# Kernel optimization log

Measured on AMD Instinct MI355X. Metric: run time of the kernel, lower is better.

The kernel has to match this reference:

```python
import jax, jax.numpy as jnp
import numpy as np

# MLA dims (DeepSeek-V3-lite style)
B, S, DIM = 1, 2048, 2048
H, NOPE, ROPE, VD, LORA = 16, 128, 64, 128, 512
QK_HEAD = NOPE + ROPE  # 192
SCALE = QK_HEAD ** -0.5
EPS = 1e-6


def _rmsnorm(x, w):
    return x * jax.lax.rsqrt(jnp.mean(x * x, axis=-1, keepdims=True) + EPS) * w


def _apply_rope(x, cos, sin):
    # x: [b, s, h, d] with interleaved (real, imag) pairs; cos/sin: [s, d//2]
    x0, x1 = x[..., 0::2], x[..., 1::2]
    c = cos[None, :, None, :]
    s = sin[None, :, None, :]
    y0 = x0 * c - x1 * s
    y1 = x0 * s + x1 * c
    return jnp.stack([y0, y1], axis=-1).reshape(x.shape)


def setup_inputs() -> dict:
    key = jax.random.key(0)
    ks = jax.random.split(key, 6)
    x = jax.random.normal(ks[0], (B, S, DIM), jnp.float32) * 0.02
    wq = jax.random.normal(ks[1], (H * QK_HEAD, DIM), jnp.float32) * 0.02
    wkv_a = jax.random.normal(ks[2], (LORA + ROPE, DIM), jnp.float32) * 0.02
    kv_norm_w = jnp.ones((LORA,), jnp.float32)
    wkv_b = jax.random.normal(ks[3], (H * (NOPE + VD), LORA), jnp.float32) * 0.02
    wo = jax.random.normal(ks[4], (DIM, H * VD), jnp.float32) * 0.02
    # rotary freqs_cis (cos/sin) for qk_rope_head_dim
    inv_freq = 1.0 / (10000.0 ** (np.arange(0, ROPE, 2, dtype=np.float32) / ROPE))
    t = np.arange(S, dtype=np.float32)
    ang = np.outer(t, inv_freq)  # [S, ROPE//2]
    cos = jnp.asarray(np.cos(ang), jnp.float32)
    sin = jnp.asarray(np.sin(ang), jnp.float32)
    return {"x": x, "cos": cos, "sin": sin, "wq": wq, "wkv_a": wkv_a,
            "kv_norm_w": kv_norm_w, "wkv_b": wkv_b, "wo": wo}


def reference(x, cos, sin, wq, wkv_a, kv_norm_w, wkv_b, wo):
    b, s, _ = x.shape
    # queries
    q = (x @ wq.T).reshape(b, s, H, QK_HEAD)
    q_nope, q_pe = q[..., :NOPE], q[..., NOPE:]
    q_pe = _apply_rope(q_pe, cos, sin)  # [b,s,h,rope]
    # latent kv
    kv = x @ wkv_a.T  # [b,s,lora+rope]
    kv_c, k_pe = kv[..., :LORA], kv[..., LORA:]
    k_pe = _apply_rope(k_pe[:, :, None, :], cos, sin)[:, :, 0, :]  # [b,s,rope]
    kv_c = _rmsnorm(kv_c, kv_norm_w)  # latent kv cache [b,s,lora]
    # absorbed weights: wkv_b viewed as [h, nope+vd, lora]
    wkv_b_r = wkv_b.reshape(H, NOPE + VD, LORA)
    w_uk = wkv_b_r[:, :NOPE]   # [h, nope, lora]
    w_uv = wkv_b_r[:, NOPE:]   # [h, vd, lora]
    # absorb: project q_nope into latent space
    q_c = jnp.einsum('bshd,hdc->bshc', q_nope, w_uk)  # [b,s,h,lora]
    scores = (jnp.einsum('bshc,btc->bsht', q_c, kv_c)
              + jnp.einsum('bshr,btr->bsht', q_pe, k_pe)) * SCALE
    # causal mask over [s, t]
    mask = jnp.where(jnp.arange(s)[:, None] >= jnp.arange(s)[None, :], 0.0, -1e30)
    scores = scores + mask[None, :, None, :].astype(scores.dtype)
    attn = jax.nn.softmax(scores, axis=-1)
    o = jnp.einsum('bsht,btc->bshc', attn, kv_c)       # [b,s,h,lora]
    o = jnp.einsum('bshc,hdc->bshd', o, w_uv)           # [b,s,h,vd]
    out = o.reshape(b, s, H * VD) @ wo.T                # [b,s,dim]
    return out
```

## Files before the change

### kernel.cpp

```cpp
#include <hip/hip_runtime.h>
#include <hip/hip_bf16.h>
#include <math.h>

#define S_LEN 2048
#define DIM   2048
#define H_N   16
#define NOPE  128
#define ROPE  64
#define VD    128
#define LORA  512
#define D_QK  576
#define SCALE_F 0.07216878364870323f
#define EPS_F 1e-6f
#define KVF 640
#define KVS 1280

typedef short short8 __attribute__((ext_vector_type(8)));
typedef short short4v __attribute__((ext_vector_type(4)));
typedef float floatx4 __attribute__((ext_vector_type(4)));

static __device__ inline unsigned short f2bf_bits(float f) {
  union { __hip_bfloat16 h; unsigned short u; } cv;
  cv.h = __float2bfloat16(f);
  return cv.u;
}

static __device__ inline float bf2f(unsigned short b) {
  union { unsigned u; float f; } cv;
  cv.u = (unsigned)b << 16;
  return cv.f;
}

static __device__ inline void gload_lds16(const short* gptr, short* lds_base_uniform) {
  __builtin_amdgcn_global_load_lds(
      (const __attribute__((address_space(1))) void*)gptr,
      (__attribute__((address_space(3))) void*)lds_base_uniform, 16, 0, 0);
}

__global__ __launch_bounds__(256) void cast_f32_bf16(
    const float* __restrict__ src, short* __restrict__ dst, int n8) {
  int i = blockIdx.x * 256 + threadIdx.x;
  if (i < n8) {
    float4 a = ((const float4*)src)[2 * i];
    float4 b = ((const float4*)src)[2 * i + 1];
    uint4 o;
    o.x = (unsigned)f2bf_bits(a.x) | ((unsigned)f2bf_bits(a.y) << 16);
    o.y = (unsigned)f2bf_bits(a.z) | ((unsigned)f2bf_bits(a.w) << 16);
    o.z = (unsigned)f2bf_bits(b.x) | ((unsigned)f2bf_bits(b.y) << 16);
    o.w = (unsigned)f2bf_bits(b.z) | ((unsigned)f2bf_bits(b.w) << 16);
    ((uint4*)dst)[i] = o;
  }
}

__global__ __launch_bounds__(256) void zero_short8(short* __restrict__ dst, int n8) {
  int i = blockIdx.x * 256 + threadIdx.x;
  if (i < n8) ((uint4*)dst)[i] = (uint4){0u, 0u, 0u, 0u};
}

__global__ __launch_bounds__(256) void transpose_wuk(
    const float* __restrict__ wkvb, short* __restrict__ wukT) {
  __shared__ float tile[32][33];
  const int h = blockIdx.z, c0 = blockIdx.y * 32, d0 = blockIdx.x * 32;
  const int t = threadIdx.x;
  const int r = t >> 3, c4 = (t & 7) * 4;
  float4 v = *(const float4*)(wkvb + ((long)h * 256 + d0 + r) * 512 + c0 + c4);
  tile[r][c4 + 0] = v.x; tile[r][c4 + 1] = v.y;
  tile[r][c4 + 2] = v.z; tile[r][c4 + 3] = v.w;
  __syncthreads();
  uint2 o;
  o.x = (unsigned)f2bf_bits(tile[c4 + 0][r]) | ((unsigned)f2bf_bits(tile[c4 + 1][r]) << 16);
  o.y = (unsigned)f2bf_bits(tile[c4 + 2][r]) | ((unsigned)f2bf_bits(tile[c4 + 3][r]) << 16);
  *(uint2*)(wukT + ((long)h * 512 + c0 + r) * 128 + d0 + c4) = o;
}

__global__ __launch_bounds__(256) void gemm_bf16_nt(
    const short* __restrict__ A, const short* __restrict__ B, void* __restrict__ Cv,
    int K, int lda, int ldb, int ldc, long aB, long bB, long cB, int bf16out) {
  A += (long)blockIdx.z * aB;
  B += (long)blockIdx.z * bB;
  const int m0 = blockIdx.y * 128, n0 = blockIdx.x * 128;
  __shared__ short As[2][128 * 32];
  __shared__ short Bs[2][128 * 32];
  const int tid = threadIdx.x, w = tid >> 6, lane = tid & 63;
  const int ln = lane & 15, g = lane >> 4;
  const int mw = (w & 1) * 64, nw = (w >> 1) * 64;
  floatx4 acc[4][4];
#pragma unroll
  for (int i = 0; i < 4; ++i)
#pragma unroll
    for (int j = 0; j < 4; ++j) acc[i][j] = (floatx4){0.f, 0.f, 0.f, 0.f};

#define GEMM_STAGE(k0_, b_)                                                    \
  {                                                                            \
    _Pragma("unroll")                                                          \
    for (int i = 0; i < 2; ++i) {                                              \
      const int bc = (i * 4 + w) * 64;                                         \
      const int c = bc + lane;                                                 \
      const int row = c >> 2, quar = c & 3;                                    \
      gload_lds16(A + (long)(m0 + row) * lda + (k0_) + quar * 8, As[b_] + bc * 8); \
      gload_lds16(B + (long)(n0 + row) * ldb + (k0_) + quar * 8, Bs[b_] + bc * 8); \
    }                                                                          \
  }

  GEMM_STAGE(0, 0);
  __syncthreads();
  const int nk = K >> 5;
  for (int kt = 0; kt < nk; ++kt) {
    const int cb = kt & 1;
    if (kt + 1 < nk) GEMM_STAGE((kt + 1) << 5, cb ^ 1);
    short8 af[4], bf_[4];
#pragma unroll
    for (int mi = 0; mi < 4; ++mi)
      af[mi] = *(const short8*)(As[cb] + (mw + mi * 16 + ln) * 32 + g * 8);
#pragma unroll
    for (int ni = 0; ni < 4; ++ni)
      bf_[ni] = *(const short8*)(Bs[cb] + (nw + ni * 16 + ln) * 32 + g * 8);
#pragma unroll
    for (int mi = 0; mi < 4; ++mi)
#pragma unroll
      for (int ni = 0; ni < 4; ++ni)
        acc[mi][ni] = __builtin_amdgcn_mfma_f32_16x16x32_bf16(af[mi], bf_[ni], acc[mi][ni], 0, 0, 0);
    __syncthreads();
  }
#undef GEMM_STAGE
  if (bf16out) {
    short* Cs = (short*)Cv + (long)blockIdx.z * cB;
#pragma unroll
    for (int mi = 0; mi < 4; ++mi)
#pragma unroll
      for (int ni = 0; ni < 4; ++ni)
#pragma unroll
        for (int r = 0; r < 4; ++r)
          Cs[(long)(m0 + mw + mi * 16 + g * 4 + r) * ldc + n0 + nw + ni * 16 + ln] =
              (short)f2bf_bits(acc[mi][ni][r]);
  } else {
    float* C = (float*)Cv + (long)blockIdx.z * cB;
#pragma unroll
    for (int mi = 0; mi < 4; ++mi)
#pragma unroll
      for (int ni = 0; ni < 4; ++ni)
#pragma unroll
        for (int r = 0; r < 4; ++r)
          C[(long)(m0 + mw + mi * 16 + g * 4 + r) * ldc + n0 + nw + ni * 16 + ln] = acc[mi][ni][r];
  }
}

__global__ __launch_bounds__(64) void prep_kernel(
    float* kv, const short* __restrict__ qbufb, short* __restrict__ qhatb,
    const float* __restrict__ cosp, const float* __restrict__ sinp,
    const float* __restrict__ normw) {
  const int s = blockIdx.x;
  const int l = threadIdx.x;
  float* row = kv + (long)s * KVF;
  short* krow = (short*)kv + (long)s * KVS;

  float4 v0 = *(const float4*)(row + l * 8);
  float4 v1 = *(const float4*)(row + l * 8 + 4);
  float rx0 = 0.f, rx1 = 0.f, rc = 0.f, rs = 0.f;
  if (l < 32) {
    rc = cosp[s * 32 + l];
    rs = sinp[s * 32 + l];
    rx0 = row[512 + 2 * l];
    rx1 = row[512 + 2 * l + 1];
  }
  float4 w0 = *(const float4*)(normw + l * 8);
  float4 w1 = *(const float4*)(normw + l * 8 + 4);

  float ss = v0.x * v0.x + v0.y * v0.y + v0.z * v0.z + v0.w * v0.w +
             v1.x * v1.x + v1.y * v1.y + v1.z * v1.z + v1.w * v1.w;
#pragma unroll
  for (int off = 32; off; off >>= 1) ss += __shfl_xor(ss, off, 64);
  const float scale = rsqrtf(ss * (1.0f / (float)LORA) + EPS_F);
  v0.x *= scale * w0.x; v0.y *= scale * w0.y; v0.z *= scale * w0.z; v0.w *= scale * w0.w;
  v1.x *= scale * w1.x; v1.y *= scale * w1.y; v1.z *= scale * w1.z; v1.w *= scale * w1.w;

  uint4 pk;
  pk.x = (unsigned)f2bf_bits(v0.x) | ((unsigned)f2bf_bits(v0.y) << 16);
  pk.y = (unsigned)f2bf_bits(v0.z) | ((unsigned)f2bf_bits(v0.w) << 16);
  pk.z = (unsigned)f2bf_bits(v1.x) | ((unsigned)f2bf_bits(v1.y) << 16);
  pk.w = (unsigned)f2bf_bits(v1.z) | ((unsigned)f2bf_bits(v1.w) << 16);
  *(uint4*)(krow + l * 8) = pk;

  if (l < 32) {
    const float y0 = rx0 * rc - rx1 * rs;
    const float y1 = rx0 * rs + rx1 * rc;
    unsigned pr = (unsigned)f2bf_bits(y0) | ((unsigned)f2bf_bits(y1) << 16);
    *(unsigned*)(krow + 512 + 2 * l) = pr;
  }

#pragma unroll
  for (int it = 0; it < 8; ++it) {
    const int p = it * 64 + l;
    const int h = p >> 5;
    const int i = p & 31;
    const float c = cosp[s * 32 + i];
    const float sn = sinp[s * 32 + i];
    const short* qp = qbufb + (long)s * 3072 + h * 192 + NOPE;
    const unsigned uq = *(const unsigned*)(qp + 2 * i);
    const float x0 = bf2f((unsigned short)uq);
    const float x1 = bf2f((unsigned short)(uq >> 16));
    const float y0 = x0 * c - x1 * sn;
    const float y1 = x0 * sn + x1 * c;
    short* dst = qhatb + ((long)h * S_LEN + s) * D_QK + 512;
    *(unsigned*)(dst + 2 * i) = (unsigned)f2bf_bits(y0) | ((unsigned)f2bf_bits(y1) << 16);
  }
}

__global__ __launch_bounds__(256) void transpose_v(
    const short* __restrict__ kbf, short* __restrict__ kvt) {
  __shared__ short tile[32][36];
  const int d0 = blockIdx.x * 32;
  const int s0 = blockIdx.y * 32;
  const int t = threadIdx.x;
  const int r = t >> 3;
  const int c4 = (t & 7) * 4;
  uint2 v = *(const uint2*)(kbf + (long)(s0 + r) * KVS + d0 + c4);
  *(uint2*)(&tile[r][c4]) = v;
  __syncthreads();
  uint2 o;
  o.x = (unsigned)(unsigned short)tile[c4 + 0][r] | ((unsigned)(unsigned short)tile[c4 + 1][r] << 16);
  o.y = (unsigned)(unsigned short)tile[c4 + 2][r] | ((unsigned)(unsigned short)tile[c4 + 3][r] << 16);
  *(uint2*)(kvt + (long)(d0 + r) * S_LEN + s0 + c4) = o;
}

__global__ __launch_bounds__(256) void build_ktt(
    const short* __restrict__ kbf, short* __restrict__ ktt) {
  const int kt = blockIdx.x;
  for (int idx = threadIdx.x; idx < 18 * 64; idx += 256) {
    const int c = idx >> 6, l = idx & 63;
    const int ln = l & 15, g = l >> 4;
    uint4 v = *(const uint4*)(kbf + (long)(kt * 16 + ln) * KVS + c * 32 + g * 8);
    *(uint4*)(ktt + ((long)(kt * 18 + c) * 64 + l) * 8) = v;
  }
}

__global__ __launch_bounds__(256) void build_vtt(
    const short* __restrict__ kvt, short* __restrict__ vtt) {
  const int kt = blockIdx.x;
  for (int idx = threadIdx.x; idx < 32 * 64; idx += 256) {
    const int nt = idx >> 6, l = idx & 63;
    const int ln = l & 15, g = l >> 4;
    uint4 v = *(const uint4*)(kvt + (long)(nt * 16 + ln) * S_LEN + kt * 32 + g * 8);
    *(uint4*)(vtt + ((long)(kt * 32 + nt) * 64 + l) * 8) = v;
  }
}

__global__ __launch_bounds__(256, 2) void flash_reg(
    const short* __restrict__ qhat,
    const short* __restrict__ ktt,
    const short* __restrict__ vtt,
    short* __restrict__ obuf) {
  const int bid = blockIdx.x;
  const int hp = bid & 7;
  const int v = bid >> 3;
  const int vi = v & 31, vj = v >> 5;
  const int qw = (vj == 0) ? 127 - vi : (vj == 1) ? 64 + vi : (vj == 2) ? 63 - vi : vi;
  const int q0 = qw * 16;
  const int tid = threadIdx.x;
  const int w = tid >> 6;
  const int lane = tid & 63;
  const int ln = lane & 15, g = lane >> 4;
  const int hh = w & 1;
  const int h = hp * 2 + hh;
  const int dh = w >> 1;
  const int vbase = dh * 256;
  const int qlim = q0 + ln;

  __shared__ short Kt[2][36 * 64 * 8];
  __shared__ __align__(16) short Pl[2][2][16][40];
  __shared__ float Ls[4][16];

  short8 qfr[18];
  {
    const short* qrow = qhat + ((long)h * S_LEN + q0 + ln) * D_QK;
#pragma unroll
    for (int c = 0; c < 18; ++c)
      qfr[c] = *(const short8*)(qrow + c * 32 + g * 8);
  }

  floatx4 oacc[16];
#pragma unroll
  for (int nt = 0; nt < 16; ++nt) oacc[nt] = (floatx4){0.f, 0.f, 0.f, 0.f};
  float lsum = 0.f;

  const int npairs = (qw + 2) >> 1;

#define FL_STAGE(pair_, b_)                                                    \
  {                                                                            \
    const short* ksrc_ = ktt + (long)(pair_) * (36 * 512);                     \
    _Pragma("unroll")                                                          \
    for (int i = 0; i < 9; ++i) {                                              \
      const int grp = i * 4 + w;                                               \
      gload_lds16(ksrc_ + (long)(grp * 64 + lane) * 8, Kt[b_] + grp * 512);    \
    }                                                                          \
  }

#define FL_PV(pp_, par_)                                                       \
  {                                                                            \
    const short8 pb8 = *(const short8*)(&Pl[par_][hh][ln][g * 8]);             \
    const short* vp = vtt + (((long)(pp_) * 32 + dh * 16) * 64 + lane) * 8;    \
    _Pragma("unroll")                                                          \
    for (int half = 0; half < 2; ++half) {                                     \
      short8 va[8];                                                            \
      _Pragma("unroll")                                                        \
      for (int j = 0; j < 8; ++j)                                              \
        va[j] = *(const short8*)(vp + (half * 8 + j) * 512);                   \
      __builtin_amdgcn_s_setprio(1);                                           \
      _Pragma("unroll")                                                        \
      for (int j = 0; j < 8; ++j)                                              \
        oacc[half * 8 + j] = __builtin_amdgcn_mfma_f32_16x16x32_bf16(          \
            va[j], pb8, oacc[half * 8 + j], 0, 0, 0);                          \
      __builtin_amdgcn_s_setprio(0);                                           \
    }                                                                          \
  }

  FL_STAGE(0, 0);
  __syncthreads();

  for (int p = 0; p < npairs; ++p) {
    const int cb = p & 1;
    if (p + 1 < npairs) FL_STAGE(p + 1, cb ^ 1);
    const int t0 = p * 32;
    const short* kb = Kt[cb] + dh * (18 * 512);
    floatx4 s0 = (floatx4){0.f, 0.f, 0.f, 0.f};
    floatx4 s1 = (floatx4){0.f, 0.f, 0.f, 0.f};
    __builtin_amdgcn_s_setprio(1);
#pragma unroll
    for (int c = 0; c < 18; c += 2) {
      short8 k0 = *(const short8*)(kb + (c * 64 + lane) * 8);
      short8 k1 = *(const short8*)(kb + ((c + 1) * 64 + lane) * 8);
      s0 = __builtin_amdgcn_mfma_f32_16x16x32_bf16(k0, qfr[c], s0, 0, 0, 0);
      s1 = __builtin_amdgcn_mfma_f32_16x16x32_bf16(k1, qfr[c + 1], s1, 0, 0, 0);
    }
    __builtin_amdgcn_s_setprio(0);
    short4v p4;
    float psum = 0.f;
#pragma unroll
    for (int r = 0; r < 4; ++r) {
      const int ki = t0 + dh * 16 + g * 4 + r;
      float sc = fminf(fmaxf((s0[r] + s1[r]) * SCALE_F, -30.f), 30.f);
      float pv_ = (ki <= qlim) ? __expf(sc) : 0.f;
      psum += pv_;
      p4[r] = (short)f2bf_bits(pv_);
    }
    lsum += psum;
    union { short4v s; unsigned long long u; } upk;
    upk.s = p4;
    *(unsigned long long*)(&Pl[cb][hh][ln][dh * 16 + g * 4]) = upk.u;
    if (p > 0) FL_PV(p - 1, cb ^ 1);
    __syncthreads();
  }
  FL_PV(npairs - 1, (npairs - 1) & 1);
#undef FL_PV
#undef FL_STAGE

  lsum += __shfl_xor(lsum, 16, 64);
  lsum += __shfl_xor(lsum, 32, 64);
  if (g == 0) Ls[w][ln] = lsum;
  __syncthreads();
  lsum += Ls[w ^ 2][ln];
  const float inv = 1.0f / fmaxf(lsum, 1e-30f);

  short* orow = obuf + ((long)h * S_LEN + q0 + ln) * 512 + vbase + g * 4;
#pragma unroll
  for (int nt = 0; nt < 16; ++nt) {
    unsigned lo = (unsigned)f2bf_bits(oacc[nt][0] * inv) | ((unsigned)f2bf_bits(oacc[nt][1] * inv) << 16);
    unsigned hi = (unsigned)f2bf_bits(oacc[nt][2] * inv) | ((unsigned)f2bf_bits(oacc[nt][3] * inv) << 16);
    unsigned long long st = (unsigned long long)lo | ((unsigned long long)hi << 32);
    *(unsigned long long*)(orow + nt * 16) = st;
  }
}

extern "C" void kernel_launch(void* const* d_in, const int* in_sizes, int n_in,
                              void* d_out, int out_size, void* d_ws, size_t ws_size,
                              hipStream_t stream) {
  (void)in_sizes; (void)n_in; (void)out_size; (void)ws_size;
  const float* x      = (const float*)d_in[0];
  const float* cosp   = (const float*)d_in[1];
  const float* sinp   = (const float*)d_in[2];
  const float* wq     = (const float*)d_in[3];
  const float* wkv_a  = (const float*)d_in[4];
  const float* normw  = (const float*)d_in[5];
  const float* wkv_b  = (const float*)d_in[6];
  const float* wo     = (const float*)d_in[7];
  float* out = (float*)d_out;

  float* ws = (float*)d_ws;
  float* qbufR  = ws;
  float* kvold  = qbufR + (long)S_LEN * 3072;
  float* qhatR  = kvold + (long)S_LEN * D_QK;
  float* obufR  = qhatR + (long)H_N * S_LEN * D_QK;
  float* oprojR = obufR + (long)H_N * S_LEN * LORA;

  float* kvpad = oprojR;
  short* kbf = (short*)kvpad;
  short* wkvap = (short*)kvold;

  short* qbufb = (short*)qbufR;
  short* kvt = qbufb + (long)S_LEN * 3072;
  short* ktt = kvt + (long)512 * S_LEN;
  short* vtt = ktt + (long)128 * 18 * 64 * 8;

  short* qhatb  = (short*)qhatR;
  short* wkvbb  = qhatb + (long)H_N * S_LEN * D_QK;
  short* oprojb = wkvbb + (long)4096 * 512;
  short* wob    = oprojb + (long)2048 * 2048;

  short* xb   = (short*)obufR;
  short* wqb  = xb  + (long)2048 * 2048;
  short* wukT = wqb + (long)3072 * 2048;
  short* obufb = (short*)obufR;

  cast_f32_bf16<<<dim3(2048), 256, 0, stream>>>(x, xb, 2048 * 2048 / 8);
  cast_f32_bf16<<<dim3(3072), 256, 0, stream>>>(wq, wqb, 3072 * 2048 / 8);
  cast_f32_bf16<<<dim3(576), 256, 0, stream>>>(wkv_a, wkvap, 576 * 2048 / 8);
  zero_short8<<<dim3(64), 256, 0, stream>>>(wkvap + 576L * 2048, 64 * 2048 / 8);

  gemm_bf16_nt<<<dim3(3072 / 128, 2048 / 128, 1), 256, 0, stream>>>(
      xb, wqb, qbufb, 2048, 2048, 2048, 3072, 0, 0, 0, 1);

  gemm_bf16_nt<<<dim3(KVF / 128, 2048 / 128, 1), 256, 0, stream>>>(
      xb, wkvap, kvpad, 2048, 2048, 2048, KVF, 0, 0, 0, 0);

  prep_kernel<<<dim3(S_LEN), 64, 0, stream>>>(kvpad, qbufb, qhatb, cosp, sinp, normw);

  transpose_wuk<<<dim3(4, 16, 16), 256, 0, stream>>>(wkv_b, wukT);

  gemm_bf16_nt<<<dim3(512 / 128, 2048 / 128, 16), 256, 0, stream>>>(
      qbufb, wukT, qhatb, 128, 3072, 128, 576,
      192L, 512L * 128, (long)S_LEN * D_QK, 1);

  transpose_v<<<dim3(16, 64), 256, 0, stream>>>(kbf, kvt);
  build_ktt<<<dim3(128), 256, 0, stream>>>(kbf, ktt);
  build_vtt<<<dim3(64), 256, 0, stream>>>(kvt, vtt);

  flash_reg<<<dim3(1024), 256, 0, stream>>>(qhatb, ktt, vtt, obufb);

  cast_f32_bf16<<<dim3(1024), 256, 0, stream>>>(wkv_b, wkvbb, 4096 * 512 / 8);

  gemm_bf16_nt<<<dim3(1, 2048 / 128, 16), 256, 0, stream>>>(
      obufb, wkvbb + 128L * 512, oprojb, 512, 512, 512, 2048,
      (long)S_LEN * 512, 256L * 512, 128L, 1);

  cast_f32_bf16<<<dim3(2048), 256, 0, stream>>>(wo, wob, 2048 * 2048 / 8);
  gemm_bf16_nt<<<dim3(2048 / 128, 2048 / 128, 1), 256, 0, stream>>>(
      oprojb, wob, out, 2048, 2048, 2048, 2048, 0, 0, 0, 0);
}
```

Measured before the change: 452.3 us.

## Share staged K/V across two query tiles per block and stage V in LDS

The flash attention kernel now runs 512-thread blocks, each covering two 16-row query tiles (32 rows) for a head pair. Both tiles share one LDS copy of each K pair. V tiles are also staged into double-buffered LDS with async loads, where before each wave read them straight from global memory. The aim is to halve the global and L2 traffic for K and V and to keep V reads off the critical global-latency path. In exchange, LDS use per block roughly doubles to about 137KB, which likely limits each CU to one block, and the grid shrinks to 512 blocks with coarser causal load balancing.

Measured after the change: 454.2 us. Within noise of the previous version (+0.4%).

```diff
diff --git a/kernel.cpp b/kernel.cpp
--- a/kernel.cpp
+++ b/kernel.cpp
@@ -245,7 +245,7 @@
   }
 }
 
-__global__ __launch_bounds__(256, 2) void flash_reg(
+__global__ __launch_bounds__(512, 2) void flash_reg(
     const short* __restrict__ qhat,
     const short* __restrict__ ktt,
     const short* __restrict__ vtt,
@@ -254,28 +254,30 @@
   const int hp = bid & 7;
   const int v = bid >> 3;
   const int vi = v & 31, vj = v >> 5;
-  const int qw = (vj == 0) ? 127 - vi : (vj == 1) ? 64 + vi : (vj == 2) ? 63 - vi : vi;
-  const int q0 = qw * 16;
+  const int qt2 = (vj == 0) ? 63 - vi : vi;
+  const int q0 = qt2 * 32;
   const int tid = threadIdx.x;
   const int w = tid >> 6;
   const int lane = tid & 63;
   const int ln = lane & 15, g = lane >> 4;
   const int hh = w & 1;
+  const int dh = (w >> 1) & 1;
+  const int qt = w >> 2;
   const int h = hp * 2 + hh;
-  const int dh = w >> 1;
-  const int vbase = dh * 256;
-  const int qlim = q0 + ln;
-
-  __shared__ short Kt[2][36 * 64 * 8];
-  __shared__ __align__(16) short Pl[2][2][16][40];
-  __shared__ float Ls[4][16];
+  const int qrow = q0 + qt * 16 + ln;
+  const int qlim = qrow;
+
+  __shared__ short Kt[2][36 * 512];
+  __shared__ short Vt[2][32 * 512];
+  __shared__ __align__(16) short Pl[2][2][2][16][40];
+  __shared__ float Ls[8][16];
 
   short8 qfr[18];
   {
-    const short* qrow = qhat + ((long)h * S_LEN + q0 + ln) * D_QK;
+    const short* qr = qhat + ((long)h * S_LEN + qrow) * D_QK;
 #pragma unroll
     for (int c = 0; c < 18; ++c)
-      qfr[c] = *(const short8*)(qrow + c * 32 + g * 8);
+      qfr[c] = *(const short8*)(qr + c * 32 + g * 8);
   }
 
   floatx4 oacc[16];
@@ -283,28 +285,39 @@
   for (int nt = 0; nt < 16; ++nt) oacc[nt] = (floatx4){0.f, 0.f, 0.f, 0.f};
   float lsum = 0.f;
 
-  const int npairs = (qw + 2) >> 1;
-
-#define FL_STAGE(pair_, b_)                                                    \
+  const int npairs = qt2 + 1;
+
+#define FL_STAGEK(pair_, b_)                                                   \
   {                                                                            \
-    const short* ksrc_ = ktt + (long)(pair_) * (36 * 512);                     \
+    const short* ks_ = ktt + (long)(pair_) * (36 * 512);                       \
     _Pragma("unroll")                                                          \
-    for (int i = 0; i < 9; ++i) {                                              \
-      const int grp = i * 4 + w;                                               \
-      gload_lds16(ksrc_ + (long)(grp * 64 + lane) * 8, Kt[b_] + grp * 512);    \
+    for (int i = 0; i < 5; ++i) {                                              \
+      const int grp = i * 8 + w;                                               \
+      if (grp < 36)                                                            \
+        gload_lds16(ks_ + (long)(grp * 64 + lane) * 8, Kt[b_] + grp * 512);    \
     }                                                                          \
   }
 
-#define FL_PV(pp_, par_)                                                       \
+#define FL_STAGEV(pair_, b_)                                                   \
   {                                                                            \
-    const short8 pb8 = *(const short8*)(&Pl[par_][hh][ln][g * 8]);             \
-    const short* vp = vtt + (((long)(pp_) * 32 + dh * 16) * 64 + lane) * 8;    \
+    const short* vs_ = vtt + (long)(pair_) * (32 * 512);                       \
+    _Pragma("unroll")                                                          \
+    for (int i = 0; i < 4; ++i) {                                              \
+      const int grp = i * 8 + w;                                               \
+      gload_lds16(vs_ + (long)(grp * 64 + lane) * 8, Vt[b_] + grp * 512);      \
+    }                                                                          \
+  }
+
+#define FL_PV(par_)                                                            \
+  {                                                                            \
+    const short8 pb8 = *(const short8*)(&Pl[par_][hh][qt][ln][g * 8]);         \
+    const short* vb_ = Vt[par_] + dh * (16 * 512);                             \
     _Pragma("unroll")                                                          \
     for (int half = 0; half < 2; ++half) {                                     \
       short8 va[8];                                                            \
       _Pragma("unroll")                                                        \
       for (int j = 0; j < 8; ++j)                                              \
-        va[j] = *(const short8*)(vp + (half * 8 + j) * 512);                   \
+        va[j] = *(const short8*)(vb_ + (half * 8 + j) * 512 + lane * 8);       \
       __builtin_amdgcn_s_setprio(1);                                           \
       _Pragma("unroll")                                                        \
       for (int j = 0; j < 8; ++j)                                              \
@@ -314,13 +327,13 @@
     }                                                                          \
   }
 
-  FL_STAGE(0, 0);
+  FL_STAGEK(0, 0);
   __syncthreads();
 
   for (int p = 0; p < npairs; ++p) {
     const int cb = p & 1;
-    if (p + 1 < npairs) FL_STAGE(p + 1, cb ^ 1);
-    const int t0 = p * 32;
+    if (p + 1 < npairs) FL_STAGEK(p + 1, cb ^ 1);
+    FL_STAGEV(p, cb);
     const short* kb = Kt[cb] + dh * (18 * 512);
     floatx4 s0 = (floatx4){0.f, 0.f, 0.f, 0.f};
     floatx4 s1 = (floatx4){0.f, 0.f, 0.f, 0.f};
@@ -337,7 +350,7 @@
     float psum = 0.f;
 #pragma unroll
     for (int r = 0; r < 4; ++r) {
-      const int ki = t0 + dh * 16 + g * 4 + r;
+      const int ki = p * 32 + dh * 16 + g * 4 + r;
       float sc = fminf(fmaxf((s0[r] + s1[r]) * SCALE_F, -30.f), 30.f);
       float pv_ = (ki <= qlim) ? __expf(sc) : 0.f;
       psum += pv_;
@@ -346,13 +359,14 @@
     lsum += psum;
     union { short4v s; unsigned long long u; } upk;
     upk.s = p4;
-    *(unsigned long long*)(&Pl[cb][hh][ln][dh * 16 + g * 4]) = upk.u;
-    if (p > 0) FL_PV(p - 1, cb ^ 1);
+    *(unsigned long long*)(&Pl[cb][hh][qt][ln][dh * 16 + g * 4]) = upk.u;
+    if (p > 0) FL_PV(cb ^ 1);
     __syncthreads();
   }
-  FL_PV(npairs - 1, (npairs - 1) & 1);
+  FL_PV((npairs - 1) & 1);
 #undef FL_PV
-#undef FL_STAGE
+#undef FL_STAGEV
+#undef FL_STAGEK
 
   lsum += __shfl_xor(lsum, 16, 64);
   lsum += __shfl_xor(lsum, 32, 64);
@@ -361,7 +375,7 @@
   lsum += Ls[w ^ 2][ln];
   const float inv = 1.0f / fmaxf(lsum, 1e-30f);
 
-  short* orow = obuf + ((long)h * S_LEN + q0 + ln) * 512 + vbase + g * 4;
+  short* orow = obuf + ((long)h * S_LEN + qrow) * 512 + dh * 256 + g * 4;
 #pragma unroll
   for (int nt = 0; nt < 16; ++nt) {
     unsigned lo = (unsigned)f2bf_bits(oacc[nt][0] * inv) | ((unsigned)f2bf_bits(oacc[nt][1] * inv) << 16);
@@ -434,7 +448,7 @@
   build_ktt<<<dim3(128), 256, 0, stream>>>(kbf, ktt);
   build_vtt<<<dim3(64), 256, 0, stream>>>(kvt, vtt);
 
-  flash_reg<<<dim3(1024), 256, 0, stream>>>(qhatb, ktt, vtt, obufb);
+  flash_reg<<<dim3(512), 512, 0, stream>>>(qhatb, ktt, vtt, obufb);
 
   cast_f32_bf16<<<dim3(1024), 256, 0, stream>>>(wkv_b, wkvbb, 4096 * 512 / 8);
 
```
